# Kernel optimization log

Measured on AMD Instinct MI355X. Metric: run time of the kernel, lower is better.

The kernel has to match this reference:

```python
import jax, jax.numpy as jnp
import numpy as np

DIM, HEADS, K_MAX, K_MIN = 512, 8, 32, 4
DH = DIM // HEADS


def _conv1x1(x, w, b=None):
    # 1x1 Conv2d == pointwise linear over channels: [B,C,H,W] x [O,C] -> [B,O,H,W]
    y = jnp.einsum('bchw,oc->bohw', x, w)
    if b is not None:
        y = y + b[None, :, None, None]
    return y


def setup_inputs() -> dict:
    key = jax.random.key(0)
    ks = jax.random.split(key, 8)
    B, C, H, W = 2, DIM, 64, 64
    s = lambda fan: 1.0 / np.sqrt(fan)
    x = jax.random.normal(ks[0], (B, C, H, W), jnp.float32)
    w_qkv = jax.random.normal(ks[1], (3 * C, C), jnp.float32) * s(C)   # qkv conv, bias=False
    w_proj = jax.random.normal(ks[2], (C, C), jnp.float32) * s(C)      # proj conv
    b_proj = jax.random.normal(ks[3], (C,), jnp.float32) * s(C)
    w_g1 = jax.random.normal(ks[4], (C // 4, C), jnp.float32) * s(C)   # gate conv 1
    b_g1 = jax.random.normal(ks[5], (C // 4,), jnp.float32) * s(C)
    w_g2 = jax.random.normal(ks[6], (1, C // 4), jnp.float32) * s(C // 4)  # gate conv 2
    b_g2 = jnp.full((1,), -1.0, jnp.float32)  # nn.init.constant_(gate[-2].bias, -1.0)
    return {"x": x, "w_qkv": w_qkv, "w_proj": w_proj, "b_proj": b_proj,
            "w_g1": w_g1, "b_g1": b_g1, "w_g2": w_g2, "b_g2": b_g2}


def reference(x, w_qkv, w_proj, b_proj, w_g1, b_g1, w_g2, b_g2):
    B, C, H, W = x.shape
    N = H * W
    qkv = _conv1x1(x, w_qkv)                              # [B,3C,H,W]
    q, k, v = jnp.split(qkv, 3, axis=1)

    def rs(t):  # [B,C,H,W] -> [B,heads,N,dh]
        return t.reshape(B, HEADS, DH, N).transpose(0, 1, 3, 2)

    q, k, v = rs(q), rs(k), rs(v)
    sim = jnp.einsum('bhid,bhjd->bhij', q, k) / np.sqrt(DH)  # [B,h,N,N]

    # adaptive tau gate -> per-query dynamic k
    tau = jax.nn.sigmoid(_conv1x1(jax.nn.relu(_conv1x1(x, w_g1, b_g1)), w_g2, b_g2))
    tau = tau.reshape(B, 1, N)
    k_dyn = jnp.clip((tau * K_MAX).astype(jnp.int32), K_MIN, K_MAX)  # [B,1,N]

    topk_val, topk_idx = jax.lax.top_k(sim, K_MAX)         # [B,h,N,K], sorted descending
    mask = jnp.arange(K_MAX)[None, None, None, :] < k_dyn[..., None]  # [B,1,N,K] (bcast over h)
    topk_val = jnp.where(mask, topk_val, -jnp.inf)
    attn = jax.nn.softmax(topk_val, axis=-1)               # [B,h,N,K]

    # gather values: gathered[b,h,i,kk,:] = v[b,h,topk_idx[b,h,i,kk],:]
    bi = jnp.arange(B)[:, None, None, None]
    hi = jnp.arange(HEADS)[None, :, None, None]
    gathered = v[bi, hi, topk_idx]                         # [B,h,N,K,dh]
    out = jnp.einsum('bhnk,bhnkd->bhnd', attn, gathered)   # [B,h,N,dh]

    out = out.transpose(0, 1, 3, 2).reshape(B, C, H, W)
    out = _conv1x1(out, w_proj, b_proj)                    # proj (proj_drop=0)
    return x + out
```

## Files before the change

kernel.cpp:

```cpp
#include <hip/hip_runtime.h>
#include <math.h>

#define XSTRIDE  2097152u
#define G1STRIDE 524288u

typedef _Float16 f16;
typedef f16   f16x8  __attribute__((ext_vector_type(8)));
typedef float f32x16 __attribute__((ext_vector_type(16)));
typedef unsigned int u32;
typedef unsigned short u16;

#define WS_QH 0u
#define WS_QL 2097152u
#define WS_KH 4194304u
#define WS_KL 6291456u
#define WS_VB 8388608u
#define WS_G1 10485760u
#define WS_KD 11534336u
#define WS_CI 11542528u

__global__ __launch_bounds__(256)
void gate1_kernel(const float* __restrict__ A,
                  const float* __restrict__ B,
                  const float* __restrict__ bias,
                  float* __restrict__ G1)
{
    const int tid = threadIdx.x;
    const int tm = tid & 15;
    const int tn = tid >> 4;
    const int n0 = blockIdx.x * 32;
    const int b  = blockIdx.z;
    const float* Bb = B + (size_t)b * XSTRIDE;

    __shared__ float As[16][132];
    __shared__ float Bs[16][34];

    float acc[8][2];
    #pragma unroll
    for (int i = 0; i < 8; ++i) { acc[i][0] = 0.0f; acc[i][1] = 0.0f; }

    for (int k0 = 0; k0 < 512; k0 += 16) {
        {
            int id = tid * 2;
            #pragma unroll
            for (int r = 0; r < 2; ++r, ++id) {
                int m = id >> 2, kq = (id & 3) * 4;
                float4 v = *(const float4*)(A + (size_t)m * 512 + k0 + kq);
                As[kq + 0][m] = v.x; As[kq + 1][m] = v.y;
                As[kq + 2][m] = v.z; As[kq + 3][m] = v.w;
            }
        }
        {
            int kk = tid >> 4;
            int nn = (tid & 15) * 2;
            float2 v = *(const float2*)(Bb + (size_t)(k0 + kk) * 4096 + n0 + nn);
            Bs[kk][nn] = v.x; Bs[kk][nn + 1] = v.y;
        }
        __syncthreads();
        #pragma unroll
        for (int k = 0; k < 16; ++k) {
            float4 a0 = *(const float4*)(&As[k][tm * 8]);
            float4 a1 = *(const float4*)(&As[k][tm * 8 + 4]);
            float a[8] = {a0.x, a0.y, a0.z, a0.w, a1.x, a1.y, a1.z, a1.w};
            float b0 = Bs[k][tn * 2], b1 = Bs[k][tn * 2 + 1];
            #pragma unroll
            for (int i = 0; i < 8; ++i) {
                acc[i][0] += a[i] * b0;
                acc[i][1] += a[i] * b1;
            }
        }
        __syncthreads();
    }

    #pragma unroll
    for (int i = 0; i < 8; ++i) {
        int o = tm * 8 + i;
        float bi = bias[o];
        float* dst = G1 + (size_t)b * G1STRIDE + (size_t)o * 4096 + n0 + tn * 2;
        dst[0] = fmaxf(acc[i][0] + bi, 0.0f);
        dst[1] = fmaxf(acc[i][1] + bi, 0.0f);
    }
}

__global__ __launch_bounds__(256)
void convert_kernel(const float* __restrict__ x,
                    f16* __restrict__ XTH, f16* __restrict__ XTL)
{
    __shared__ float T[64][65];
    const int b = blockIdx.z;
    const int n0 = blockIdx.x * 64, k0 = blockIdx.y * 64;
    const int tid = threadIdx.x;
    const float* xb = x + (size_t)b * XSTRIDE;

    {
        const int c = tid & 63, r = tid >> 6;
        #pragma unroll
        for (int i = 0; i < 16; ++i)
            T[r + i * 4][c] = xb[(size_t)(k0 + r + i * 4) * 4096 + n0 + c];
    }
    __syncthreads();
    const int n = tid >> 2, a = tid & 3;
    f16x8 vh[2], vl[2];
    #pragma unroll
    for (int p = 0; p < 2; ++p)
        #pragma unroll
        for (int j = 0; j < 8; ++j) {
            float v = T[a * 16 + p * 8 + j][n];
            f16 h = (f16)v;
            vh[p][j] = h;
            vl[p][j] = (f16)((v - (float)h) * 4096.0f);
        }
    size_t dst = ((size_t)(b * 4096) + n0 + n) * 512 + k0 + a * 16;
    *(f16x8*)(XTH + dst)     = vh[0];
    *(f16x8*)(XTH + dst + 8) = vh[1];
    *(f16x8*)(XTL + dst)     = vl[0];
    *(f16x8*)(XTL + dst + 8) = vl[1];
}

__global__ __launch_bounds__(256, 2)
void qkv_gemm(const float* __restrict__ W, const f16* __restrict__ XTH,
              const f16* __restrict__ XTL,
              f16* __restrict__ QH, f16* __restrict__ QL,
              f16* __restrict__ KH, f16* __restrict__ KL,
              f16* __restrict__ VB)
{
    __shared__ __align__(16) char smem[33792];
    f16* Ah = (f16*)smem;
    f16* Al = (f16*)(smem + 6144);
    f16* Bh = (f16*)(smem + 12288);
    f16* Bl = (f16*)(smem + 18432);

    const int tid  = threadIdx.x;
    const int wid  = tid >> 6, lane = tid & 63;
    const int ln   = lane & 31, g = lane >> 5;
    const int wm   = wid >> 1, wn = wid & 1;
    const int m0   = blockIdx.y * 128;
    const int n0   = blockIdx.x * 128;
    const int b    = blockIdx.z;

    const int sm = tid >> 1, sko = (tid & 1) * 8;
    const float* wsrc  = W + (size_t)(m0 + sm) * 512 + sko;
    const f16*  bsrcH = XTH + ((size_t)(b * 4096) + n0 + sm) * 512 + sko;
    const f16*  bsrcL = XTL + ((size_t)(b * 4096) + n0 + sm) * 512 + sko;

    f32x16 accH[2][2], accL[2][2];
    #pragma unroll
    for (int rb = 0; rb < 2; ++rb)
        #pragma unroll
        for (int cb = 0; cb < 2; ++cb)
            #pragma unroll
            for (int r = 0; r < 16; ++r) { accH[rb][cb][r] = 0.0f; accL[rb][cb][r] = 0.0f; }

    for (int k0 = 0; k0 < 512; k0 += 16) {
        {
            float4 v0 = *(const float4*)(wsrc + k0);
            float4 v1 = *(const float4*)(wsrc + k0 + 4);
            float vv[8] = {v0.x, v0.y, v0.z, v0.w, v1.x, v1.y, v1.z, v1.w};
            f16x8 hh, ll;
            #pragma unroll
            for (int j = 0; j < 8; ++j) {
                f16 h = (f16)vv[j];
                hh[j] = h;
                ll[j] = (f16)((vv[j] - (float)h) * 4096.0f);
            }
            *(f16x8*)(Ah + sm * 24 + sko) = hh;
            *(f16x8*)(Al + sm * 24 + sko) = ll;
            *(f16x8*)(Bh + sm * 24 + sko) = *(const f16x8*)(bsrcH + k0);
            *(f16x8*)(Bl + sm * 24 + sko) = *(const f16x8*)(bsrcL + k0);
        }
        __syncthreads();
        f16x8 a_h[2], a_l[2], b_h[2], b_l[2];
        #pragma unroll
        for (int rb = 0; rb < 2; ++rb) {
            int row = wm * 64 + rb * 32 + ln;
            a_h[rb] = *(const f16x8*)(Ah + row * 24 + g * 8);
            a_l[rb] = *(const f16x8*)(Al + row * 24 + g * 8);
        }
        #pragma unroll
        for (int cb = 0; cb < 2; ++cb) {
            int col = wn * 64 + cb * 32 + ln;
            b_h[cb] = *(const f16x8*)(Bh + col * 24 + g * 8);
            b_l[cb] = *(const f16x8*)(Bl + col * 24 + g * 8);
        }
        #pragma unroll
        for (int rb = 0; rb < 2; ++rb)
            #pragma unroll
            for (int cb = 0; cb < 2; ++cb) {
                accH[rb][cb] = __builtin_amdgcn_mfma_f32_32x32x16_f16(a_h[rb], b_h[cb], accH[rb][cb], 0, 0, 0);
                accL[rb][cb] = __builtin_amdgcn_mfma_f32_32x32x16_f16(a_h[rb], b_l[cb], accL[rb][cb], 0, 0, 0);
                accL[rb][cb] = __builtin_amdgcn_mfma_f32_32x32x16_f16(a_l[rb], b_h[cb], accL[rb][cb], 0, 0, 0);
            }
        __syncthreads();
    }

    const int which = m0 >> 9;
    const float scale = (which == 0) ? 0.125f : 1.0f;
    const int hh_ = ((m0 & 511) >> 6) + wm;
    const size_t rowb0 = (size_t)(b * 8 + hh_) * 4096 + n0 + wn * 64 + lane;
    float* E = (float*)smem + wid * 2112;

    #pragma unroll
    for (int rb = 0; rb < 2; ++rb) {
        #pragma unroll
        for (int cb = 0; cb < 2; ++cb)
            #pragma unroll
            for (int r = 0; r < 16; ++r) {
                int row = (r & 3) + 8 * (r >> 2) + 4 * g;
                E[row * 66 + cb * 32 + ln] =
                    accH[rb][cb][r] + accL[rb][cb][r] * (1.0f / 4096.0f);
            }
        __syncthreads();
        const int dbase = rb * 32;
        if (which == 2) {
            #pragma unroll
            for (int oct = 0; oct < 4; ++oct) {
                f16x8 vv;
                #pragma unroll
                for (int j = 0; j < 8; ++j) vv[j] = (f16)E[(oct * 8 + j) * 66 + lane];
                *(f16x8*)(VB + rowb0 * 64 + dbase + oct * 8) = vv;
            }
        } else {
            f16* DH = which ? KH : QH;
            f16* DL = which ? KL : QL;
            #pragma unroll
            for (int oct = 0; oct < 4; ++oct) {
                f16x8 vh, vl;
                #pragma unroll
                for (int j = 0; j < 8; ++j) {
                    float xx = E[(oct * 8 + j) * 66 + lane] * scale;
                    f16 h = (f16)xx;
                    vh[j] = h;
                    vl[j] = (f16)((xx - (float)h) * 4096.0f);
                }
                *(f16x8*)(DH + rowb0 * 64 + dbase + oct * 8) = vh;
                *(f16x8*)(DL + rowb0 * 64 + dbase + oct * 8) = vl;
            }
        }
        __syncthreads();
    }
}

__global__ __launch_bounds__(256, 2)
void proj_gemm(const float* __restrict__ W, const f16* __restrict__ OH,
               const f16* __restrict__ OL, const float* __restrict__ bias,
               const float* __restrict__ resid, float* __restrict__ out)
{
    __shared__ __align__(16) char smem[33792];
    f16* Ah = (f16*)smem;
    f16* Al = (f16*)(smem + 6144);
    f16* Bh = (f16*)(smem + 12288);
    f16* Bl = (f16*)(smem + 18432);

    const int tid  = threadIdx.x;
    const int wid  = tid >> 6, lane = tid & 63;
    const int ln   = lane & 31, g = lane >> 5;
    const int wm   = wid >> 1, wn = wid & 1;
    const int m0   = blockIdx.y * 128;
    const int n0   = blockIdx.x * 128;
    const int b    = blockIdx.z;

    const int sm = tid >> 1, sko = (tid & 1) * 8;
    const float* wsrc  = W + (size_t)(m0 + sm) * 512 + sko;
    const f16*  bsrcH = OH + ((size_t)(b * 4096) + n0 + sm) * 512 + sko;
    const f16*  bsrcL = OL + ((size_t)(b * 4096) + n0 + sm) * 512 + sko;

    f32x16 accH[2][2], accL[2][2];
    #pragma unroll
    for (int rb = 0; rb < 2; ++rb)
        #pragma unroll
        for (int cb = 0; cb < 2; ++cb)
            #pragma unroll
            for (int r = 0; r < 16; ++r) { accH[rb][cb][r] = 0.0f; accL[rb][cb][r] = 0.0f; }

    for (int k0 = 0; k0 < 512; k0 += 16) {
        {
            float4 v0 = *(const float4*)(wsrc + k0);
            float4 v1 = *(const float4*)(wsrc + k0 + 4);
            float vv[8] = {v0.x, v0.y, v0.z, v0.w, v1.x, v1.y, v1.z, v1.w};
            f16x8 hh, ll;
            #pragma unroll
            for (int j = 0; j < 8; ++j) {
                f16 h = (f16)vv[j];
                hh[j] = h;
                ll[j] = (f16)((vv[j] - (float)h) * 4096.0f);
            }
            *(f16x8*)(Ah + sm * 24 + sko) = hh;
            *(f16x8*)(Al + sm * 24 + sko) = ll;
            *(f16x8*)(Bh + sm * 24 + sko) = *(const f16x8*)(bsrcH + k0);
            *(f16x8*)(Bl + sm * 24 + sko) = *(const f16x8*)(bsrcL + k0);
        }
        __syncthreads();
        f16x8 a_h[2], a_l[2], b_h[2], b_l[2];
        #pragma unroll
        for (int rb = 0; rb < 2; ++rb) {
            int row = wm * 64 + rb * 32 + ln;
            a_h[rb] = *(const f16x8*)(Ah + row * 24 + g * 8);
            a_l[rb] = *(const f16x8*)(Al + row * 24 + g * 8);
        }
        #pragma unroll
        for (int cb = 0; cb < 2; ++cb) {
            int col = wn * 64 + cb * 32 + ln;
            b_h[cb] = *(const f16x8*)(Bh + col * 24 + g * 8);
            b_l[cb] = *(const f16x8*)(Bl + col * 24 + g * 8);
        }
        #pragma unroll
        for (int rb = 0; rb < 2; ++rb)
            #pragma unroll
            for (int cb = 0; cb < 2; ++cb) {
                accH[rb][cb] = __builtin_amdgcn_mfma_f32_32x32x16_f16(a_h[rb], b_h[cb], accH[rb][cb], 0, 0, 0);
                accL[rb][cb] = __builtin_amdgcn_mfma_f32_32x32x16_f16(a_h[rb], b_l[cb], accL[rb][cb], 0, 0, 0);
                accL[rb][cb] = __builtin_amdgcn_mfma_f32_32x32x16_f16(a_l[rb], b_h[cb], accL[rb][cb], 0, 0, 0);
            }
        __syncthreads();
    }

    float* E = (float*)smem + wid * 2112;
    #pragma unroll
    for (int rb = 0; rb < 2; ++rb) {
        #pragma unroll
        for (int cb = 0; cb < 2; ++cb)
            #pragma unroll
            for (int r = 0; r < 16; ++r) {
                int row = (r & 3) + 8 * (r >> 2) + 4 * g;
                E[row * 66 + cb * 32 + ln] =
                    accH[rb][cb][r] + accL[rb][cb][r] * (1.0f / 4096.0f);
            }
        __syncthreads();
        #pragma unroll 4
        for (int r = 0; r < 32; ++r) {
            int o = m0 + wm * 64 + rb * 32 + r;
            size_t off = (size_t)b * XSTRIDE + (size_t)o * 4096
                       + n0 + wn * 64 + lane;
            out[off] = E[r * 66 + lane] + bias[o] + resid[off];
        }
        __syncthreads();
    }
}

__global__ __launch_bounds__(64)
void gate2_kernel(const float* __restrict__ G1, const float* __restrict__ w2,
                  const float* __restrict__ b2, int* __restrict__ KD)
{
    const int b = blockIdx.y;
    const int n = blockIdx.x * 64 + threadIdx.x;
    const float* g = G1 + (size_t)b * G1STRIDE + n;
    float z = b2[0];
    #pragma unroll 8
    for (int c = 0; c < 128; ++c) z += w2[c] * g[(size_t)c * 4096];
    float tau = 1.0f / (1.0f + expf(-z));
    int kd = (int)(tau * 32.0f);
    kd = min(32, max(4, kd));
    KD[b * 4096 + n] = kd;
}

#define LOAD_BF(B0,B1,B2,B3,B4,B5,B6,B7, KHP, KLP, CB) do {                   \
    const f16* _ph = (KHP) + (size_t)((CB) * 32 + ln) * 64 + g * 8;           \
    const f16* _pl = (KLP) + (size_t)((CB) * 32 + ln) * 64 + g * 8;           \
    B0 = *(const f16x8*)(_ph);      B1 = *(const f16x8*)(_ph + 16);           \
    B2 = *(const f16x8*)(_ph + 32); B3 = *(const f16x8*)(_ph + 48);           \
    B4 = *(const f16x8*)(_pl);      B5 = *(const f16x8*)(_pl + 16);           \
    B6 = *(const f16x8*)(_pl + 32); B7 = *(const f16x8*)(_pl + 48);           \
} while (0)

#define P1_SCAN() do {                                                        \
    u32 _m = 0;                                                               \
    _Pragma("unroll")                                                         \
    for (int _q = 0; _q < 16; ++_q) {                                         \
        float2 _v = *(const float2*)(srow + 2 * _q);                          \
        _m |= (_v.x > thr) ? (1u << (2 * _q)) : 0u;                           \
        _m |= (_v.y > thr) ? (1u << (2 * _q + 1)) : 0u;                       \
    }                                                                         \
    while (__ballot(_m != 0u)) {                                              \
        bool _act = (_m != 0u);                                               \
        int _j = __builtin_ctz(_m ? _m : 1u);                                 \
        float _c = _act ? srow[_j] : 0.0f;                                    \
        _m &= (_m - 1u);                                                      \
        if (_act && _c > thr) {                                               \
            _Pragma("unroll")                                                 \
            for (int _r = 31; _r >= 1; --_r)                                  \
                L[_r] = __builtin_amdgcn_fmed3f(_c, L[_r - 1], L[_r]);        \
            L[0] = fmaxf(L[0], _c);                                           \
        }                                                                     \
    }                                                                         \
    {                                                                         \
        float _th = L[31];                                                    \
        _Pragma("unroll")                                                     \
        for (int _r = 30; _r >= 0; --_r) _th = (kdm1 == _r) ? L[_r] : _th;    \
        thr = _th;                                                            \
    }                                                                         \
} while (0)

#define P2_SCAN(JBASE) do {                                                   \
    u32 _m = 0;                                                               \
    _Pragma("unroll")                                                         \
    for (int _q = 0; _q < 16; ++_q) {                                         \
        float2 _v = *(const float2*)(srow + 2 * _q);                          \
        _m |= (_v.x >= theta) ? (1u << (2 * _q)) : 0u;                        \
        _m |= (_v.y >= theta) ? (1u << (2 * _q + 1)) : 0u;                    \
    }                                                                         \
    while (__ballot(_m != 0u)) {                                              \
        bool _act = (_m != 0u);                                               \
        int _j = __builtin_ctz(_m ? _m : 1u);                                 \
        float _c = _act ? srow[_j] : 0.0f;                                    \
        _m &= (_m - 1u);                                                      \
        if (_act) {                                                           \
            bool _isGT = _c > theta;                                          \
            bool _doA = (_isGT || eqc < eqNeed) && cnt < 32;                  \
            if (_doA) {                                                       \
                cvp[cnt] = _c;                                                \
                cip[cnt] = (u16)((JBASE) + _j);                               \
                cnt++;                                                        \
                if (!_isGT) eqc++;                                            \
            }                                                                 \
        }                                                                     \
    }                                                                         \
} while (0)

__device__ __forceinline__ void score_from(
    f16x8 bh0, f16x8 bh1, f16x8 bh2, f16x8 bh3,
    f16x8 bl0, f16x8 bl1, f16x8 bl2, f16x8 bl3,
    const f16x8 ah[2][4], const f16x8 al[2][4],
    float* __restrict__ Ss, int ln, int g)
{
    __builtin_amdgcn_s_setprio(1);
    #pragma unroll
    for (int rb = 0; rb < 2; ++rb) {
        f32x16 acc, accL;
        #pragma unroll
        for (int r = 0; r < 16; ++r) { acc[r] = 0.0f; accL[r] = 0.0f; }
        acc  = __builtin_amdgcn_mfma_f32_32x32x16_f16(ah[rb][0], bh0, acc,  0, 0, 0);
        accL = __builtin_amdgcn_mfma_f32_32x32x16_f16(al[rb][0], bh0, accL, 0, 0, 0);
        accL = __builtin_amdgcn_mfma_f32_32x32x16_f16(ah[rb][0], bl0, accL, 0, 0, 0);
        acc  = __builtin_amdgcn_mfma_f32_32x32x16_f16(ah[rb][1], bh1, acc,  0, 0, 0);
        accL = __builtin_amdgcn_mfma_f32_32x32x16_f16(al[rb][1], bh1, accL, 0, 0, 0);
        accL = __builtin_amdgcn_mfma_f32_32x32x16_f16(ah[rb][1], bl1, accL, 0, 0, 0);
        acc  = __builtin_amdgcn_mfma_f32_32x32x16_f16(ah[rb][2], bh2, acc,  0, 0, 0);
        accL = __builtin_amdgcn_mfma_f32_32x32x16_f16(al[rb][2], bh2, accL, 0, 0, 0);
        accL = __builtin_amdgcn_mfma_f32_32x32x16_f16(ah[rb][2], bl2, accL, 0, 0, 0);
        acc  = __builtin_amdgcn_mfma_f32_32x32x16_f16(ah[rb][3], bh3, acc,  0, 0, 0);
        accL = __builtin_amdgcn_mfma_f32_32x32x16_f16(al[rb][3], bh3, accL, 0, 0, 0);
        accL = __builtin_amdgcn_mfma_f32_32x32x16_f16(ah[rb][3], bl3, accL, 0, 0, 0);
        #pragma unroll
        for (int r = 0; r < 16; ++r) {
            int riw = rb * 32 + (r & 3) + 8 * (r >> 2) + 4 * g;
            Ss[riw * 34 + ln] = acc[r] + accL[r] * (1.0f / 4096.0f);
        }
    }
    __builtin_amdgcn_s_setprio(0);
}

__global__ __launch_bounds__(64)
__attribute__((amdgpu_waves_per_eu(2, 2)))
void select_kernel(const f16* __restrict__ QH, const f16* __restrict__ QL,
                   const f16* __restrict__ KH, const f16* __restrict__ KL,
                   const int* __restrict__ KD,
                   float* __restrict__ CV, u16* __restrict__ CI)
{
    const int qt = blockIdx.x >> 1;
    const int hf = blockIdx.x & 1;
    const int h = blockIdx.y, b = blockIdx.z;
    const size_t base = (size_t)((b * 8 + h) * 4096) * 64;
    const int lane = threadIdx.x;
    const int ln = lane & 31, g = lane >> 5;
    const int nw = qt * 64;
    const int k0base = hf * 2048;

    const int kd = KD[b * 4096 + nw + lane];
    const int kdm1 = kd - 1;

    __shared__ float Ss[64 * 34];

    f16x8 ah[2][4], al[2][4];
    #pragma unroll
    for (int rb = 0; rb < 2; ++rb) {
        const f16* ph = QH + base + (size_t)(nw + rb * 32 + ln) * 64 + g * 8;
        const f16* pl = QL + base + (size_t)(nw + rb * 32 + ln) * 64 + g * 8;
        #pragma unroll
        for (int s = 0; s < 4; ++s) {
            ah[rb][s] = *(const f16x8*)(ph + s * 16);
            al[rb][s] = *(const f16x8*)(pl + s * 16);
        }
    }

    const float INF = __builtin_inff();
    const float* srow = &Ss[lane * 34];

    f16x8 c0, c1, c2, c3, c4, c5, c6, c7;
    f16x8 n0, n1, n2, n3, n4, n5, n6, n7;

    float L[32];
    #pragma unroll
    for (int r = 0; r < 32; ++r) L[r] = -INF;
    float thr = -INF;

    {
        const f16* kh0 = KH + base + (size_t)k0base * 64;
        const f16* kl0 = KL + base + (size_t)k0base * 64;
        LOAD_BF(c0, c1, c2, c3, c4, c5, c6, c7, kh0, kl0, 0);
        for (int t = 0; t < 32; ++t) {
            const f16* kh_t = KH + base + (size_t)(k0base + t * 64) * 64;
            const f16* kl_t = KL + base + (size_t)(k0base + t * 64) * 64;
            const int t1 = (t < 31) ? t + 1 : 31;
            const f16* kh_n = KH + base + (size_t)(k0base + t1 * 64) * 64;
            const f16* kl_n = KL + base + (size_t)(k0base + t1 * 64) * 64;
            LOAD_BF(n0, n1, n2, n3, n4, n5, n6, n7, kh_t, kl_t, 1);
            score_from(c0, c1, c2, c3, c4, c5, c6, c7, ah, al, Ss, ln, g);
            P1_SCAN();
            LOAD_BF(c0, c1, c2, c3, c4, c5, c6, c7, kh_n, kl_n, 0);
            score_from(n0, n1, n2, n3, n4, n5, n6, n7, ah, al, Ss, ln, g);
            P1_SCAN();
        }
    }
    const float theta = thr;
    int cntGT = 0;
    #pragma unroll
    for (int r = 0; r < 32; ++r) cntGT += ((r < kd) && (L[r] > theta)) ? 1 : 0;
    const int eqNeed = kd - cntGT;

    const size_t crow = (size_t)((b * 8 + h) * 4096 + nw + lane);
    float* cvp = CV + crow * 64 + hf * 32;
    u16*   cip = CI + crow * 64 + hf * 32;
    int cnt = 0, eqc = 0;

    {
        const f16* kh0 = KH + base + (size_t)k0base * 64;
        const f16* kl0 = KL + base + (size_t)k0base * 64;
        LOAD_BF(c0, c1, c2, c3, c4, c5, c6, c7, kh0, kl0, 0);
        for (int t = 0; t < 32; ++t) {
            const f16* kh_t = KH + base + (size_t)(k0base + t * 64) * 64;
            const f16* kl_t = KL + base + (size_t)(k0base + t * 64) * 64;
            const int t1 = (t < 31) ? t + 1 : 31;
            const f16* kh_n = KH + base + (size_t)(k0base + t1 * 64) * 64;
            const f16* kl_n = KL + base + (size_t)(k0base + t1 * 64) * 64;
            LOAD_BF(n0, n1, n2, n3, n4, n5, n6, n7, kh_t, kl_t, 1);
            score_from(c0, c1, c2, c3, c4, c5, c6, c7, ah, al, Ss, ln, g);
            P2_SCAN(k0base + t * 64);
            LOAD_BF(c0, c1, c2, c3, c4, c5, c6, c7, kh_n, kl_n, 0);
            score_from(n0, n1, n2, n3, n4, n5, n6, n7, ah, al, Ss, ln, g);
            P2_SCAN(k0base + t * 64 + 32);
        }
    }
}

__global__ __launch_bounds__(64)
void merge_kernel(const float* __restrict__ CV, const u16* __restrict__ CI,
                  const int* __restrict__ KD, const f16* __restrict__ VB,
                  f16* __restrict__ OH, f16* __restrict__ OL)
{
    const int tid = threadIdx.x;
    const size_t R0 = (size_t)blockIdx.x * 64;

    __shared__ float Lv[64][66];
    __shared__ u16   Li[64][66];
    __shared__ float Mv[64][34];
    __shared__ u16   Mi[64][34];

    for (int i = 0; i < 64; ++i) {
        Lv[i][tid] = CV[(R0 + i) * 64 + tid];
        Li[i][tid] = CI[(R0 + i) * 64 + tid];
    }
    __syncthreads();

    const int myR = (int)R0 + tid;
    const int b = myR >> 15, n = myR & 4095, h = (myR >> 12) & 7;
    const int kd = KD[b * 4096 + n];

    const float INF = __builtin_inff();
    float L[32]; int I[32];
    #pragma unroll
    for (int r = 0; r < 32; ++r) { L[r] = -INF; I[r] = 0; }

    for (int i = 0; i < 64; ++i) {
        float c = Lv[tid][i];
        int  ix = Li[tid][i];
        if (c > L[31]) {
            #pragma unroll
            for (int r = 31; r >= 1; --r) {
                bool gp = c > L[r - 1];
                bool gc = c > L[r];
                L[r] = gp ? L[r - 1] : (gc ? c : L[r]);
                I[r] = gp ? I[r - 1] : (gc ? ix : I[r]);
            }
            if (c > L[0]) { I[0] = ix; L[0] = c; }
        }
    }

    #pragma unroll
    for (int r = 0; r < 32; ++r) { Mv[tid][r] = L[r]; Mi[tid][r] = (u16)I[r]; }

    const float mx = Mv[tid][0];
    float sum = 0.0f;
    for (int k = 0; k < kd; ++k) {
        float e = expf(Mv[tid][k] - mx);
        Mv[tid][k] = e;
        sum += e;
    }
    const float inv = 1.0f / sum;

    float o[64];
    #pragma unroll
    for (int d = 0; d < 64; ++d) o[d] = 0.0f;
    const size_t vbase = (size_t)((b * 8 + h)) * 4096 * 64;
    for (int k = 0; k < kd; ++k) {
        float wgt = Mv[tid][k] * inv;
        const f16* vp = VB + vbase + (size_t)Mi[tid][k] * 64;
        #pragma unroll
        for (int part = 0; part < 8; ++part) {
            f16x8 vv = *(const f16x8*)(vp + part * 8);
            #pragma unroll
            for (int e2 = 0; e2 < 8; ++e2) o[part * 8 + e2] += wgt * (float)vv[e2];
        }
    }

    const size_t obase = ((size_t)(b * 4096) + n) * 512 + h * 64;
    #pragma unroll
    for (int part = 0; part < 8; ++part) {
        f16x8 vh, vl;
        #pragma unroll
        for (int e2 = 0; e2 < 8; ++e2) {
            float v = o[part * 8 + e2];
            f16 hh = (f16)v;
            vh[e2] = hh;
            vl[e2] = (f16)((v - (float)hh) * 4096.0f);
        }
        *(f16x8*)(OH + obase + part * 8) = vh;
        *(f16x8*)(OL + obase + part * 8) = vl;
    }
}

extern "C" void kernel_launch(void* const* d_in, const int* in_sizes, int n_in,
                              void* d_out, int out_size, void* d_ws, size_t ws_size,
                              hipStream_t stream)
{
    const float* x      = (const float*)d_in[0];
    const float* w_qkv  = (const float*)d_in[1];
    const float* w_proj = (const float*)d_in[2];
    const float* b_proj = (const float*)d_in[3];
    const float* w_g1   = (const float*)d_in[4];
    const float* b_g1   = (const float*)d_in[5];
    const float* w_g2   = (const float*)d_in[6];
    const float* b_g2   = (const float*)d_in[7];
    float* out = (float*)d_out;
    float* ws  = (float*)d_ws;

    f16* QH = (f16*)(ws + WS_QH);
    f16* QL = (f16*)(ws + WS_QL);
    f16* KH = (f16*)(ws + WS_KH);
    f16* KL = (f16*)(ws + WS_KL);
    f16* VB = (f16*)(ws + WS_VB);
    float* G1 = ws + WS_G1;
    int*   KD = (int*)(ws + WS_KD);
    u16*   CI = (u16*)(ws + WS_CI);
    float* CV = out;
    f16* OH = (f16*)QH;
    f16* OL = (f16*)QL;

    f16* XTH = (f16*)out;
    f16* XTL = (f16*)out + 4194304;

    convert_kernel<<<dim3(64, 8, 2), 256, 0, stream>>>(x, XTH, XTL);
    qkv_gemm<<<dim3(32, 12, 2), 256, 0, stream>>>(
        w_qkv, XTH, XTL, QH, QL, KH, KL, VB);
    gate1_kernel<<<dim3(128, 1, 2), 256, 0, stream>>>(w_g1, x, b_g1, G1);

    hipMemsetAsync(CV, 0xFF, (size_t)out_size * sizeof(float), stream);

    gate2_kernel<<<dim3(64, 2), 64, 0, stream>>>(G1, w_g2, b_g2, KD);
    select_kernel<<<dim3(128, 8, 2), 64, 0, stream>>>(QH, QL, KH, KL, KD, CV, CI);
    merge_kernel<<<dim3(1024), 64, 0, stream>>>(CV, CI, KD, VB, OH, OL);
    proj_gemm<<<dim3(32, 4, 2), 256, 0, stream>>>(
        w_proj, OH, OL, b_proj, x, out);
}
```

Before: 605.9 us.

## Split select key range across two waves with shared-memory top-k merge

Each select block now runs two waves, and each wave scans half of the block's 2048-key range. After pass 1 the two waves exchange their sorted top-32 lists through shared memory and merge them with a bitonic-style network to get a common threshold. They then split the output slots, including the tie quota, so that pass 2 can write candidates without overlap. This doubles the parallelism per query tile and shortens the serial key loop, at the cost of a barrier, the merge work, and changed occupancy hints.

```diff
diff --git a/kernel.cpp b/kernel.cpp
--- a/kernel.cpp
+++ b/kernel.cpp
@@ -390,7 +390,7 @@
     }                                                                         \
 } while (0)
 
-#define P2_SCAN(JBASE) do {                                                   \
+#define P2_SCANQ(JBASE) do {                                                  \
     u32 _m = 0;                                                               \
     _Pragma("unroll")                                                         \
     for (int _q = 0; _q < 16; ++_q) {                                         \
@@ -405,10 +405,10 @@
         _m &= (_m - 1u);                                                      \
         if (_act) {                                                           \
             bool _isGT = _c > theta;                                          \
-            bool _doA = (_isGT || eqc < eqNeed) && cnt < 32;                  \
+            bool _doA = (_isGT || eqc < eqNeedW) && cnt < capW;               \
             if (_doA) {                                                       \
-                cvp[cnt] = _c;                                                \
-                cip[cnt] = (u16)((JBASE) + _j);                               \
+                cvp[slotBase + cnt] = _c;                                     \
+                cip[slotBase + cnt] = (u16)((JBASE) + _j);                    \
                 cnt++;                                                        \
                 if (!_isGT) eqc++;                                            \
             }                                                                 \
@@ -449,8 +449,8 @@
     __builtin_amdgcn_s_setprio(0);
 }
 
-__global__ __launch_bounds__(64)
-__attribute__((amdgpu_waves_per_eu(2, 2)))
+__global__ __launch_bounds__(128)
+__attribute__((amdgpu_waves_per_eu(3, 4)))
 void select_kernel(const f16* __restrict__ QH, const f16* __restrict__ QL,
                    const f16* __restrict__ KH, const f16* __restrict__ KL,
                    const int* __restrict__ KD,
@@ -460,15 +460,19 @@
     const int hf = blockIdx.x & 1;
     const int h = blockIdx.y, b = blockIdx.z;
     const size_t base = (size_t)((b * 8 + h) * 4096) * 64;
-    const int lane = threadIdx.x;
+    const int tid = threadIdx.x;
+    const int wv = tid >> 6;
+    const int lane = tid & 63;
     const int ln = lane & 31, g = lane >> 5;
     const int nw = qt * 64;
-    const int k0base = hf * 2048;
+    const int k0base = hf * 2048 + wv * 1024;
 
     const int kd = KD[b * 4096 + nw + lane];
     const int kdm1 = kd - 1;
 
-    __shared__ float Ss[64 * 34];
+    __shared__ float Ss2[2][64 * 34];
+    float* Ss = Ss2[wv];
+    const float* srow = &Ss[lane * 34];
 
     f16x8 ah[2][4], al[2][4];
     #pragma unroll
@@ -483,7 +487,6 @@
     }
 
     const float INF = __builtin_inff();
-    const float* srow = &Ss[lane * 34];
 
     f16x8 c0, c1, c2, c3, c4, c5, c6, c7;
     f16x8 n0, n1, n2, n3, n4, n5, n6, n7;
@@ -494,15 +497,15 @@
     float thr = -INF;
 
     {
-        const f16* kh0 = KH + base + (size_t)k0base * 64;
-        const f16* kl0 = KL + base + (size_t)k0base * 64;
-        LOAD_BF(c0, c1, c2, c3, c4, c5, c6, c7, kh0, kl0, 0);
-        for (int t = 0; t < 32; ++t) {
-            const f16* kh_t = KH + base + (size_t)(k0base + t * 64) * 64;
-            const f16* kl_t = KL + base + (size_t)(k0base + t * 64) * 64;
-            const int t1 = (t < 31) ? t + 1 : 31;
-            const f16* kh_n = KH + base + (size_t)(k0base + t1 * 64) * 64;
-            const f16* kl_n = KL + base + (size_t)(k0base + t1 * 64) * 64;
+        const f16* khQ = KH + base + (size_t)k0base * 64;
+        const f16* klQ = KL + base + (size_t)k0base * 64;
+        LOAD_BF(c0, c1, c2, c3, c4, c5, c6, c7, khQ, klQ, 0);
+        for (int t = 0; t < 16; ++t) {
+            const f16* kh_t = khQ + (size_t)(t * 64) * 64;
+            const f16* kl_t = klQ + (size_t)(t * 64) * 64;
+            const int t1 = (t < 15) ? t + 1 : 15;
+            const f16* kh_n = khQ + (size_t)(t1 * 64) * 64;
+            const f16* kl_n = klQ + (size_t)(t1 * 64) * 64;
             LOAD_BF(n0, n1, n2, n3, n4, n5, n6, n7, kh_t, kl_t, 1);
             score_from(c0, c1, c2, c3, c4, c5, c6, c7, ah, al, Ss, ln, g);
             P1_SCAN();
@@ -511,11 +514,55 @@
             P1_SCAN();
         }
     }
-    const float theta = thr;
-    int cntGT = 0;
-    #pragma unroll
-    for (int r = 0; r < 32; ++r) cntGT += ((r < kd) && (L[r] > theta)) ? 1 : 0;
-    const int eqNeed = kd - cntGT;
+
+    #pragma unroll
+    for (int r = 0; r < 32; ++r) Ss[lane * 33 + r] = L[r];
+    __syncthreads();
+    {
+        const float* oth = &Ss2[wv ^ 1][0];
+        #pragma unroll
+        for (int i = 0; i < 32; ++i)
+            L[i] = fmaxf(L[i], oth[lane * 33 + (31 - i)]);
+        #pragma unroll
+        for (int d = 16; d >= 1; d >>= 1)
+            #pragma unroll
+            for (int i = 0; i < 32; ++i)
+                if (!(i & d) && (i + d) < 32) {
+                    float a_ = L[i], b_ = L[i + d];
+                    L[i] = fmaxf(a_, b_);
+                    L[i + d] = fminf(a_, b_);
+                }
+    }
+    float theta;
+    {
+        float th = L[31];
+        #pragma unroll
+        for (int r = 30; r >= 0; --r) th = (kdm1 == r) ? L[r] : th;
+        theta = th;
+    }
+    int gtA = 0, eqA = 0, gtB = 0;
+    float A31;
+    {
+        const float* la = &Ss2[0][0];
+        const float* lb = &Ss2[1][0];
+        #pragma unroll
+        for (int r = 0; r < 32; ++r) {
+            float av = la[lane * 33 + r];
+            float bv = lb[lane * 33 + r];
+            gtA += (av > theta) ? 1 : 0;
+            eqA += (av == theta) ? 1 : 0;
+            gtB += (bv > theta) ? 1 : 0;
+        }
+        A31 = la[lane * 33 + 31];
+    }
+    __syncthreads();
+
+    const int eqNeed = kd - gtA - gtB;
+    const int eqCapA = (A31 == theta) ? eqNeed : min(eqA, eqNeed);
+    const int capA   = gtA + eqCapA;
+    const int slotBase = wv ? capA : 0;
+    const int capW     = wv ? (kd - capA) : capA;
+    const int eqNeedW  = wv ? (eqNeed - eqCapA) : eqCapA;
 
     const size_t crow = (size_t)((b * 8 + h) * 4096 + nw + lane);
     float* cvp = CV + crow * 64 + hf * 32;
@@ -523,21 +570,21 @@
     int cnt = 0, eqc = 0;
 
     {
-        const f16* kh0 = KH + base + (size_t)k0base * 64;
-        const f16* kl0 = KL + base + (size_t)k0base * 64;
-        LOAD_BF(c0, c1, c2, c3, c4, c5, c6, c7, kh0, kl0, 0);
-        for (int t = 0; t < 32; ++t) {
-            const f16* kh_t = KH + base + (size_t)(k0base + t * 64) * 64;
-            const f16* kl_t = KL + base + (size_t)(k0base + t * 64) * 64;
-            const int t1 = (t < 31) ? t + 1 : 31;
-            const f16* kh_n = KH + base + (size_t)(k0base + t1 * 64) * 64;
-            const f16* kl_n = KL + base + (size_t)(k0base + t1 * 64) * 64;
+        const f16* khQ = KH + base + (size_t)k0base * 64;
+        const f16* klQ = KL + base + (size_t)k0base * 64;
+        LOAD_BF(c0, c1, c2, c3, c4, c5, c6, c7, khQ, klQ, 0);
+        for (int t = 0; t < 16; ++t) {
+            const f16* kh_t = khQ + (size_t)(t * 64) * 64;
+            const f16* kl_t = klQ + (size_t)(t * 64) * 64;
+            const int t1 = (t < 15) ? t + 1 : 15;
+            const f16* kh_n = khQ + (size_t)(t1 * 64) * 64;
+            const f16* kl_n = klQ + (size_t)(t1 * 64) * 64;
             LOAD_BF(n0, n1, n2, n3, n4, n5, n6, n7, kh_t, kl_t, 1);
             score_from(c0, c1, c2, c3, c4, c5, c6, c7, ah, al, Ss, ln, g);
-            P2_SCAN(k0base + t * 64);
+            P2_SCANQ(k0base + t * 64);
             LOAD_BF(c0, c1, c2, c3, c4, c5, c6, c7, kh_n, kl_n, 0);
             score_from(n0, n1, n2, n3, n4, n5, n6, n7, ah, al, Ss, ln, g);
-            P2_SCAN(k0base + t * 64 + 32);
+            P2_SCANQ(k0base + t * 64 + 32);
         }
     }
 }
@@ -666,7 +713,7 @@
     hipMemsetAsync(CV, 0xFF, (size_t)out_size * sizeof(float), stream);
 
     gate2_kernel<<<dim3(64, 2), 64, 0, stream>>>(G1, w_g2, b_g2, KD);
-    select_kernel<<<dim3(128, 8, 2), 64, 0, stream>>>(QH, QL, KH, KL, KD, CV, CI);
+    select_kernel<<<dim3(128, 8, 2), 128, 0, stream>>>(QH, QL, KH, KL, KD, CV, CI);
     merge_kernel<<<dim3(1024), 64, 0, stream>>>(CV, CI, KD, VB, OH, OL);
     proj_gemm<<<dim3(32, 4, 2), 256, 0, stream>>>(
         w_proj, OH, OL, b_proj, x, out);
```

New measurement: 1.121 ms. 1.85x slower.

## Track top-k indices in the insertion list to remove the second scoring pass

Applied to the files above, without the earlier changes.

The candidate kernel used to make two full passes over all keys. The first found the per-query k-th threshold and the second recomputed the scores with MFMAs to collect indices. Now an index array is carried next to the sorted value list during the first pass, and the top-kd values and indices are written out directly. This removes half of the QK^T MFMA work and the K reloads. In exchange it adds 32 more registers and extra selects per insertion, which may hurt occupancy, and tie handling changes from the earlier eq-count logic.

```diff
diff --git a/kernel.cpp b/kernel.cpp
--- a/kernel.cpp
+++ b/kernel.cpp
@@ -362,7 +362,7 @@
     B6 = *(const f16x8*)(_pl + 32); B7 = *(const f16x8*)(_pl + 48);           \
 } while (0)
 
-#define P1_SCAN() do {                                                        \
+#define P1_SCANI(JBASE) do {                                                  \
     u32 _m = 0;                                                               \
     _Pragma("unroll")                                                         \
     for (int _q = 0; _q < 16; ++_q) {                                         \
@@ -376,10 +376,19 @@
         float _c = _act ? srow[_j] : 0.0f;                                    \
         _m &= (_m - 1u);                                                      \
         if (_act && _c > thr) {                                               \
+            int _ix = (JBASE) + _j;                                           \
             _Pragma("unroll")                                                 \
-            for (int _r = 31; _r >= 1; --_r)                                  \
+            for (int _r = 31; _r >= 1; --_r) {                                \
+                bool _gp = _c > L[_r - 1];                                    \
+                bool _gc = _c > L[_r];                                        \
+                I[_r] = _gp ? I[_r - 1] : (_gc ? _ix : I[_r]);                \
                 L[_r] = __builtin_amdgcn_fmed3f(_c, L[_r - 1], L[_r]);        \
-            L[0] = fmaxf(L[0], _c);                                           \
+            }                                                                 \
+            {                                                                 \
+                bool _g0 = _c > L[0];                                         \
+                I[0] = _g0 ? _ix : I[0];                                      \
+                L[0] = _g0 ? _c : L[0];                                       \
+            }                                                                 \
         }                                                                     \
     }                                                                         \
     {                                                                         \
@@ -387,32 +396,6 @@
         _Pragma("unroll")                                                     \
         for (int _r = 30; _r >= 0; --_r) _th = (kdm1 == _r) ? L[_r] : _th;    \
         thr = _th;                                                            \
-    }                                                                         \
-} while (0)
-
-#define P2_SCAN(JBASE) do {                                                   \
-    u32 _m = 0;                                                               \
-    _Pragma("unroll")                                                         \
-    for (int _q = 0; _q < 16; ++_q) {                                         \
-        float2 _v = *(const float2*)(srow + 2 * _q);                          \
-        _m |= (_v.x >= theta) ? (1u << (2 * _q)) : 0u;                        \
-        _m |= (_v.y >= theta) ? (1u << (2 * _q + 1)) : 0u;                    \
-    }                                                                         \
-    while (__ballot(_m != 0u)) {                                              \
-        bool _act = (_m != 0u);                                               \
-        int _j = __builtin_ctz(_m ? _m : 1u);                                 \
-        float _c = _act ? srow[_j] : 0.0f;                                    \
-        _m &= (_m - 1u);                                                      \
-        if (_act) {                                                           \
-            bool _isGT = _c > theta;                                          \
-            bool _doA = (_isGT || eqc < eqNeed) && cnt < 32;                  \
-            if (_doA) {                                                       \
-                cvp[cnt] = _c;                                                \
-                cip[cnt] = (u16)((JBASE) + _j);                               \
-                cnt++;                                                        \
-                if (!_isGT) eqc++;                                            \
-            }                                                                 \
-        }                                                                     \
     }                                                                         \
 } while (0)
 
@@ -489,8 +472,9 @@
     f16x8 n0, n1, n2, n3, n4, n5, n6, n7;
 
     float L[32];
-    #pragma unroll
-    for (int r = 0; r < 32; ++r) L[r] = -INF;
+    int   I[32];
+    #pragma unroll
+    for (int r = 0; r < 32; ++r) { L[r] = -INF; I[r] = 0; }
     float thr = -INF;
 
     {
@@ -505,39 +489,21 @@
             const f16* kl_n = KL + base + (size_t)(k0base + t1 * 64) * 64;
             LOAD_BF(n0, n1, n2, n3, n4, n5, n6, n7, kh_t, kl_t, 1);
             score_from(c0, c1, c2, c3, c4, c5, c6, c7, ah, al, Ss, ln, g);
-            P1_SCAN();
+            P1_SCANI(k0base + t * 64);
             LOAD_BF(c0, c1, c2, c3, c4, c5, c6, c7, kh_n, kl_n, 0);
             score_from(n0, n1, n2, n3, n4, n5, n6, n7, ah, al, Ss, ln, g);
-            P1_SCAN();
-        }
-    }
-    const float theta = thr;
-    int cntGT = 0;
-    #pragma unroll
-    for (int r = 0; r < 32; ++r) cntGT += ((r < kd) && (L[r] > theta)) ? 1 : 0;
-    const int eqNeed = kd - cntGT;
+            P1_SCANI(k0base + t * 64 + 32);
+        }
+    }
 
     const size_t crow = (size_t)((b * 8 + h) * 4096 + nw + lane);
     float* cvp = CV + crow * 64 + hf * 32;
     u16*   cip = CI + crow * 64 + hf * 32;
-    int cnt = 0, eqc = 0;
-
-    {
-        const f16* kh0 = KH + base + (size_t)k0base * 64;
-        const f16* kl0 = KL + base + (size_t)k0base * 64;
-        LOAD_BF(c0, c1, c2, c3, c4, c5, c6, c7, kh0, kl0, 0);
-        for (int t = 0; t < 32; ++t) {
-            const f16* kh_t = KH + base + (size_t)(k0base + t * 64) * 64;
-            const f16* kl_t = KL + base + (size_t)(k0base + t * 64) * 64;
-            const int t1 = (t < 31) ? t + 1 : 31;
-            const f16* kh_n = KH + base + (size_t)(k0base + t1 * 64) * 64;
-            const f16* kl_n = KL + base + (size_t)(k0base + t1 * 64) * 64;
-            LOAD_BF(n0, n1, n2, n3, n4, n5, n6, n7, kh_t, kl_t, 1);
-            score_from(c0, c1, c2, c3, c4, c5, c6, c7, ah, al, Ss, ln, g);
-            P2_SCAN(k0base + t * 64);
-            LOAD_BF(c0, c1, c2, c3, c4, c5, c6, c7, kh_n, kl_n, 0);
-            score_from(n0, n1, n2, n3, n4, n5, n6, n7, ah, al, Ss, ln, g);
-            P2_SCAN(k0base + t * 64 + 32);
+    #pragma unroll
+    for (int r = 0; r < 32; ++r) {
+        if (r < kd) {
+            cvp[r] = L[r];
+            cip[r] = (u16)I[r];
         }
     }
 }
```

After: 882.5 us. +45.7%, slower.
